# Optimization experiments

Measured on AMD Instinct MI355X. Metric: run time of the kernel, lower is better.

## Reference

```python
import jax, jax.numpy as jnp
import numpy as np

B, S, D, H, DFF = 2, 2048, 1024, 16, 4096
HD = D // H
EPS = 1e-5


def setup_inputs() -> dict:
    key = jax.random.key(0)
    ks = jax.random.split(key, 8)
    s = lambda fan_in: 1.0 / np.sqrt(fan_in)
    return {
        "x": jax.random.normal(ks[0], (B, S, D), jnp.float32),
        "ln1_g": jnp.ones((D,), jnp.float32),
        "ln1_b": jnp.zeros((D,), jnp.float32),
        "Wq": jax.random.normal(ks[1], (D, D), jnp.float32) * s(D),
        "Wk": jax.random.normal(ks[2], (D, D), jnp.float32) * s(D),
        "Wv": jax.random.normal(ks[3], (D, D), jnp.float32) * s(D),
        "Wo": jax.random.normal(ks[4], (D, D), jnp.float32) * s(D),
        "bo": jnp.zeros((D,), jnp.float32),
        "ln2_g": jnp.ones((D,), jnp.float32),
        "ln2_b": jnp.zeros((D,), jnp.float32),
        "W1": jax.random.normal(ks[5], (D, DFF), jnp.float32) * s(D),
        "b1": jnp.zeros((DFF,), jnp.float32),
        "W2": jax.random.normal(ks[6], (DFF, D), jnp.float32) * s(DFF),
        "b2": jnp.zeros((D,), jnp.float32),
    }


def _layernorm(x, g, b):
    mu = jnp.mean(x, axis=-1, keepdims=True)
    var = jnp.var(x, axis=-1, keepdims=True)
    return (x - mu) * jax.lax.rsqrt(var + EPS) * g + b


def reference(x, ln1_g, ln1_b, Wq, Wk, Wv, Wo, bo, ln2_g, ln2_b, W1, b1, W2, b2):
    # --- pre-LN + causal multi-head attention + residual ---
    h = _layernorm(x, ln1_g, ln1_b)
    q = (h @ Wq).reshape(B, S, H, HD).transpose(0, 2, 1, 3)  # [B,H,S,hd]
    k = (h @ Wk).reshape(B, S, H, HD).transpose(0, 2, 1, 3)
    v = (h @ Wv).reshape(B, S, H, HD).transpose(0, 2, 1, 3)
    scores = jnp.einsum("bhqd,bhkd->bhqk", q, k) / jnp.sqrt(jnp.float32(HD))
    causal = jnp.triu(jnp.ones((S, S), bool), k=1)  # True above diagonal -> masked
    scores = jnp.where(causal, -jnp.inf, scores)
    attn = jax.nn.softmax(scores, axis=-1)  # dropout is identity at inference
    ctx = jnp.einsum("bhqk,bhkd->bhqd", attn, v)
    ctx = ctx.transpose(0, 2, 1, 3).reshape(B, S, D)
    x = x + ctx @ Wo + bo
    # --- pre-LN + MLP + residual ---
    h = _layernorm(x, ln2_g, ln2_b)
    h = jax.nn.gelu(h @ W1 + b1, approximate=False)  # torch nn.GELU default = exact
    x = x + h @ W2 + b2
    return x
```

## Files before the change

### kernel.cpp

```cpp
#include <hip/hip_runtime.h>
#include <hip/hip_bf16.h>
#include <math.h>

using bf16 = __hip_bfloat16;
typedef short bf16x8 __attribute__((ext_vector_type(8)));
typedef float f32x4 __attribute__((ext_vector_type(4)));

static constexpr int B = 2, S = 2048, D = 1024, H = 16, HD = 64, DFF = 4096;
static constexpr int NR = B * S;
static constexpr int DQ = 3072;
static constexpr float EPS = 1e-5f;

__device__ __forceinline__ bf16 f2b(float v) { return __float2bfloat16(v); }

typedef __attribute__((address_space(1))) const void* gp1_t;
typedef __attribute__((address_space(3))) void* sp3_t;
__device__ __forceinline__ void gld_lds16(const bf16* g, bf16* l) {
    __builtin_amdgcn_global_load_lds((gp1_t)(const void*)g, (sp3_t)(void*)l, 16, 0, 0);
}

__global__ __launch_bounds__(256) void convT_kernel(const float* __restrict__ src,
                                                    bf16* __restrict__ dst,
                                                    int K, int N) {
    __shared__ float tile[64][65];
    const int k0 = blockIdx.x * 64, n0 = blockIdx.y * 64;
    const int tid = threadIdx.x;
    const int r = tid >> 4, c = (tid & 15) * 4;
#pragma unroll
    for (int rr = 0; rr < 64; rr += 16) {
        float4 v = *(const float4*)&src[(size_t)(k0 + r + rr) * N + n0 + c];
        tile[r + rr][c] = v.x; tile[r + rr][c + 1] = v.y;
        tile[r + rr][c + 2] = v.z; tile[r + rr][c + 3] = v.w;
    }
    __syncthreads();
    const int n = tid >> 2, ks = (tid & 3) * 16;
    union { bf16 h[16]; int4 v2[2]; } o;
#pragma unroll
    for (int i = 0; i < 16; ++i) o.h[i] = f2b(tile[ks + i][n]);
    bf16* dp = &dst[(size_t)(n0 + n) * K + k0 + ks];
    *(int4*)dp = o.v2[0];
    *(int4*)(dp + 8) = o.v2[1];
}

__global__ __launch_bounds__(256) void ln_kernel(const float* __restrict__ x,
                                                 const float* __restrict__ g,
                                                 const float* __restrict__ b,
                                                 bf16* __restrict__ out) {
    const int row = blockIdx.x;
    const int tid = threadIdx.x;
    const float4 v4 = ((const float4*)(x + (size_t)row * D))[tid];
    float v[4] = {v4.x, v4.y, v4.z, v4.w};
    float s = v[0] + v[1] + v[2] + v[3];
    float sq = v[0] * v[0] + v[1] * v[1] + v[2] * v[2] + v[3] * v[3];
#pragma unroll
    for (int off = 32; off >= 1; off >>= 1) {
        s += __shfl_xor(s, off);
        sq += __shfl_xor(sq, off);
    }
    __shared__ float ssum[4], ssq[4];
    const int wave = tid >> 6;
    if ((tid & 63) == 0) { ssum[wave] = s; ssq[wave] = sq; }
    __syncthreads();
    s = ssum[0] + ssum[1] + ssum[2] + ssum[3];
    sq = ssq[0] + ssq[1] + ssq[2] + ssq[3];
    const float mu = s * (1.0f / D);
    const float var = sq * (1.0f / D) - mu * mu;
    const float rstd = rsqrtf(var + EPS);
    bf16* orow = out + (size_t)row * D;
#pragma unroll
    for (int i = 0; i < 4; ++i) {
        const int c = tid * 4 + i;
        orow[c] = f2b((v[i] - mu) * rstd * g[c] + b[c]);
    }
}

template <int EPI>
__global__ __launch_bounds__(512) void gemm256(const bf16* __restrict__ A,
                                               const bf16* __restrict__ Bt,
                                               const float* __restrict__ bias,
                                               bf16* __restrict__ C,
                                               int M, int N, int K) {
    constexpr int ASZ = 256 * 32, BSZ = 128 * 32;
    constexpr int CST = 128 + 8;
    __shared__ __align__(16) bf16 smem[2 * (ASZ + BSZ)];

    const int Mtiles = M / 256;
    const int p = blockIdx.x;
    const int tm = p % Mtiles;
    const int tn = p / Mtiles;
    const int tid = threadIdx.x;
    const int wave = tid >> 6, lane = tid & 63;
    const int wm = wave >> 1, wn = wave & 1;
    const int quad = lane >> 4, l16 = lane & 15;

    f32x4 acc[4][4];
#pragma unroll
    for (int i = 0; i < 4; ++i)
#pragma unroll
        for (int j = 0; j < 4; ++j) acc[i][j] = (f32x4){0.f, 0.f, 0.f, 0.f};

    const int s_row = tid >> 2, s_seg = (tid & 3) * 8;
    const bf16* ApLo = A + (size_t)(tm * 256 + s_row) * K + s_seg;
    const size_t K128 = (size_t)128 * K;
    const bf16* Bp = Bt + (size_t)(tn * 128 + s_row) * K + s_seg;

    gld_lds16(ApLo, smem + tid * 8);
    gld_lds16(ApLo + K128, smem + (512 + tid) * 8);
    gld_lds16(Bp, smem + 2 * ASZ + tid * 8);
    ApLo += 32;
    Bp += 32;

    const int nk = K / 32;
    for (int kt = 0; kt < nk; ++kt) {
        const int cur = kt & 1, nxt = cur ^ 1;
        bf16* Acur = smem + cur * ASZ;
        bf16* Bcur = smem + 2 * ASZ + cur * BSZ;
        __syncthreads();
        if (kt + 1 < nk) {
            bf16* Anxt = smem + nxt * ASZ;
            bf16* Bnxt = smem + 2 * ASZ + nxt * BSZ;
            gld_lds16(ApLo, Anxt + tid * 8);
            gld_lds16(ApLo + K128, Anxt + (512 + tid) * 8);
            gld_lds16(Bp, Bnxt + tid * 8);
            ApLo += 32;
            Bp += 32;
        }

        bf16x8 aF[4], bF[4];
#pragma unroll
        for (int mt = 0; mt < 4; ++mt)
            aF[mt] = *(const bf16x8*)(Acur + (wm * 64 + mt * 16 + l16) * 32 + quad * 8);
#pragma unroll
        for (int nt = 0; nt < 4; ++nt)
            bF[nt] = *(const bf16x8*)(Bcur + (wn * 64 + nt * 16 + l16) * 32 + quad * 8);
#pragma unroll
        for (int mt = 0; mt < 4; ++mt)
#pragma unroll
            for (int nt = 0; nt < 4; ++nt)
                acc[mt][nt] = __builtin_amdgcn_mfma_f32_16x16x32_bf16(
                    aF[mt], bF[nt], acc[mt][nt], 0, 0, 0);
    }

#pragma unroll
    for (int hh = 0; hh < 2; ++hh) {
        __syncthreads();
        if ((wm >> 1) == hh) {
#pragma unroll
            for (int nt = 0; nt < 4; ++nt) {
                const int ccol = wn * 64 + nt * 16 + l16;
                float bv = 0.f;
                if (EPI == 2) bv = bias[tn * 128 + ccol];
#pragma unroll
                for (int mt = 0; mt < 4; ++mt) {
                    const int r0 = (wm & 1) * 64 + mt * 16 + quad * 4;
#pragma unroll
                    for (int j = 0; j < 4; ++j) {
                        float v = acc[mt][nt][j];
                        if (EPI == 2) {
                            v += bv;
                            v = 0.5f * v * (1.0f + erff(v * 0.70710678118654752f));
                        }
                        smem[(r0 + j) * CST + ccol] = f2b(v);
                    }
                }
            }
        }
        __syncthreads();
        bf16* crow = C + (size_t)(tm * 256 + hh * 128) * N + tn * 128;
#pragma unroll
        for (int i = 0; i < 4; ++i) {
            const int gid = i * 512 + tid;
            const int row = gid >> 4, c8 = gid & 15;
            const int4 val = *(const int4*)(smem + row * CST + c8 * 8);
            *(int4*)(crow + (size_t)row * N + c8 * 8) = val;
        }
    }
}

template <int EPI, int BN, int TPB>
__global__ __launch_bounds__(256) void gemm_bt(const bf16* __restrict__ A,
                                               const bf16* __restrict__ Bt,
                                               const float* __restrict__ bias,
                                               const float* __restrict__ res,
                                               void* __restrict__ Cv,
                                               int M, int N, int K) {
    constexpr int NTW = BN / 32;
    constexpr int ASZ = 128 * 32, BSZ = BN * 32;
    __shared__ __align__(16) bf16 smem[2 * (ASZ + BSZ)];

    const int Mtiles = M / 128;
    const int p = blockIdx.x;
    const int tm = p % Mtiles;
    const int tn0 = (p / Mtiles) * TPB;
    const int tid = threadIdx.x;
    const int wave = tid >> 6, lane = tid & 63;
    const int wm = wave >> 1, wn = wave & 1;
    const int quad = lane >> 4, l16 = lane & 15;

    const int s_row = tid >> 2, s_seg = (tid & 3) * 8;
    const size_t K64 = (size_t)64 * K;
    const int nk = K / 32;

    for (int tp = 0; tp < TPB; ++tp) {
        const int tn = tn0 + tp;
        if (tp) __syncthreads();

        f32x4 acc[4][NTW];
#pragma unroll
        for (int i = 0; i < 4; ++i)
#pragma unroll
            for (int j = 0; j < NTW; ++j) acc[i][j] = (f32x4){0.f, 0.f, 0.f, 0.f};

        const bf16* Ap = A + (size_t)(tm * 128 + s_row) * K + s_seg;
        const bf16* Bp = Bt + (size_t)(tn * BN + s_row) * K + s_seg;

        gld_lds16(Ap, smem + tid * 8);
        gld_lds16(Ap + K64, smem + (256 + tid) * 8);
        gld_lds16(Bp, smem + 2 * ASZ + tid * 8);
        if constexpr (BN == 128) gld_lds16(Bp + K64, smem + 2 * ASZ + (256 + tid) * 8);
        Ap += 32;
        Bp += 32;

        for (int kt = 0; kt < nk; ++kt) {
            const int cur = kt & 1, nxt = cur ^ 1;
            bf16* Acur = smem + cur * ASZ;
            bf16* Bcur = smem + 2 * ASZ + cur * BSZ;
            __syncthreads();
            if (kt + 1 < nk) {
                bf16* Anxt = smem + nxt * ASZ;
                bf16* Bnxt = smem + 2 * ASZ + nxt * BSZ;
                gld_lds16(Ap, Anxt + tid * 8);
                gld_lds16(Ap + K64, Anxt + (256 + tid) * 8);
                gld_lds16(Bp, Bnxt + tid * 8);
                if constexpr (BN == 128) gld_lds16(Bp + K64, Bnxt + (256 + tid) * 8);
                Ap += 32;
                Bp += 32;
            }

            bf16x8 aF[4], bF[NTW];
#pragma unroll
            for (int mt = 0; mt < 4; ++mt)
                aF[mt] = *(const bf16x8*)(Acur + (wm * 64 + mt * 16 + l16) * 32 + quad * 8);
#pragma unroll
            for (int nt = 0; nt < NTW; ++nt)
                bF[nt] = *(const bf16x8*)(Bcur + (wn * (BN / 2) + nt * 16 + l16) * 32 + quad * 8);
#pragma unroll
            for (int mt = 0; mt < 4; ++mt)
#pragma unroll
                for (int nt = 0; nt < NTW; ++nt)
                    acc[mt][nt] = __builtin_amdgcn_mfma_f32_16x16x32_bf16(
                        aF[mt], bF[nt], acc[mt][nt], 0, 0, 0);
        }

#pragma unroll
        for (int nt = 0; nt < NTW; ++nt) {
            const int col = tn * BN + wn * (BN / 2) + nt * 16 + l16;
            const float bv = bias[col];
#pragma unroll
            for (int mt = 0; mt < 4; ++mt) {
                const int row0 = tm * 128 + wm * 64 + mt * 16 + quad * 4;
#pragma unroll
                for (int j = 0; j < 4; ++j) {
                    const size_t idx = (size_t)(row0 + j) * N + col;
                    ((float*)Cv)[idx] = acc[mt][nt][j] + bv + res[idx];
                }
            }
        }
    }
}

__global__ __launch_bounds__(512) void fattn_kernel(const bf16* __restrict__ QKV,
                                                    bf16* __restrict__ ctx) {
    const int id = blockIdx.x;
    const int bh = id & 31;
    const int k = id >> 5;
    const int t = (k < 8) ? 15 - k : k - 8;
    const int b = bh >> 4, h = bh & (H - 1);
    const int tid = threadIdx.x;
    const int wave = tid >> 6, lane = tid & 63;
    const int quad = lane >> 4, l16 = lane & 15;
    const bf16* Qp = QKV + (size_t)b * S * DQ + h * HD;
    const bf16* Kp = Qp + D;
    const bf16* Vp = Qp + 2 * D;

    __shared__ __align__(16) bf16 Ks[2][64 * 64];
    __shared__ __align__(16) bf16 Vt[2][64][72];
    __shared__ __align__(16) bf16 Ps[128][76];

    const int keyA = tid >> 3, dsA = ((tid & 7) ^ (keyA & 7)) * 8;

    const int q0 = t * 128;
    const bf16* qg = Qp + (size_t)(q0 + wave * 16 + l16) * DQ + quad * 8;
    const bf16x8 aQ0 = *(const bf16x8*)(qg);
    const bf16x8 aQ1 = *(const bf16x8*)(qg + 32);

    f32x4 O[4];
#pragma unroll
    for (int nt = 0; nt < 4; ++nt) O[nt] = (f32x4){0.f, 0.f, 0.f, 0.f};
    float m[4] = {-3.0e38f, -3.0e38f, -3.0e38f, -3.0e38f};
    float l[4] = {0.f, 0.f, 0.f, 0.f};

    gld_lds16(Kp + (size_t)keyA * DQ + dsA, Ks[0] + tid * 8);
    {
        const bf16* vg = Vp + (size_t)lane * DQ + wave * 8;
        union { int4 v; bf16 hh[8]; } u;
        u.v = *(const int4*)vg;
#pragma unroll
        for (int i = 0; i < 8; ++i) Vt[0][wave * 8 + i][lane] = u.hh[i];
    }

    const int nch = 2 * t + 2;
    for (int c = 0; c < nch; ++c) {
        const int cur = c & 1, nxt = cur ^ 1;
        __syncthreads();
        union { int4 v; bf16 hh[8]; } u;
        if (c < nch - 1) {
            const int k1 = (c + 1) * 64;
            gld_lds16(Kp + (size_t)(k1 + keyA) * DQ + dsA, Ks[nxt] + tid * 8);
            u.v = *(const int4*)(Vp + (size_t)(k1 + lane) * DQ + wave * 8);
        }

        f32x4 sc[4];
#pragma unroll
        for (int nt = 0; nt < 4; ++nt) {
            const int r = nt * 16 + l16;
            const bf16x8 bK0 = *(const bf16x8*)(Ks[cur] + (r * 8 + (quad ^ (r & 7))) * 8);
            const bf16x8 bK1 = *(const bf16x8*)(Ks[cur] + (r * 8 + ((4 + quad) ^ (r & 7))) * 8);
            f32x4 z = (f32x4){0.f, 0.f, 0.f, 0.f};
            z = __builtin_amdgcn_mfma_f32_16x16x32_bf16(aQ0, bK0, z, 0, 0, 0);
            z = __builtin_amdgcn_mfma_f32_16x16x32_bf16(aQ1, bK1, z, 0, 0, 0);
            sc[nt] = z;
        }
#pragma unroll
        for (int nt = 0; nt < 4; ++nt)
#pragma unroll
            for (int j = 0; j < 4; ++j) sc[nt][j] *= 0.125f;
        if (c >= 2 * t) {
            const int kbase = (c - 2 * t) * 64;
#pragma unroll
            for (int nt = 0; nt < 4; ++nt) {
                const int rel_k = kbase + nt * 16 + l16;
#pragma unroll
                for (int j = 0; j < 4; ++j)
                    if (rel_k > wave * 16 + quad * 4 + j) sc[nt][j] = -3.0e38f;
            }
        }
        float al[4];
#pragma unroll
        for (int j = 0; j < 4; ++j) {
            float mx = fmaxf(fmaxf(sc[0][j], sc[1][j]), fmaxf(sc[2][j], sc[3][j]));
#pragma unroll
            for (int off = 1; off <= 8; off <<= 1) mx = fmaxf(mx, __shfl_xor(mx, off));
            const float mn = fmaxf(m[j], mx);
            al[j] = __expf(m[j] - mn);
            m[j] = mn;
            float rs = 0.f;
#pragma unroll
            for (int nt = 0; nt < 4; ++nt) {
                sc[nt][j] = __expf(sc[nt][j] - mn);
                rs += sc[nt][j];
            }
#pragma unroll
            for (int off = 1; off <= 8; off <<= 1) rs += __shfl_xor(rs, off);
            l[j] = l[j] * al[j] + rs;
        }
#pragma unroll
        for (int nt = 0; nt < 4; ++nt)
#pragma unroll
            for (int j = 0; j < 4; ++j)
                Ps[wave * 16 + quad * 4 + j][nt * 16 + l16] = f2b(sc[nt][j]);
        asm volatile("s_waitcnt lgkmcnt(0)" ::: "memory");
        const bf16x8 aP0 = *(const bf16x8*)&Ps[wave * 16 + l16][quad * 8];
        const bf16x8 aP1 = *(const bf16x8*)&Ps[wave * 16 + l16][32 + quad * 8];
#pragma unroll
        for (int nt = 0; nt < 4; ++nt)
#pragma unroll
            for (int j = 0; j < 4; ++j) O[nt][j] *= al[j];
#pragma unroll
        for (int nt = 0; nt < 4; ++nt) {
            const bf16x8 bV0 = *(const bf16x8*)&Vt[cur][nt * 16 + l16][quad * 8];
            const bf16x8 bV1 = *(const bf16x8*)&Vt[cur][nt * 16 + l16][32 + quad * 8];
            O[nt] = __builtin_amdgcn_mfma_f32_16x16x32_bf16(aP0, bV0, O[nt], 0, 0, 0);
            O[nt] = __builtin_amdgcn_mfma_f32_16x16x32_bf16(aP1, bV1, O[nt], 0, 0, 0);
        }
        if (c < nch - 1) {
#pragma unroll
            for (int i = 0; i < 8; ++i) Vt[nxt][wave * 8 + i][lane] = u.hh[i];
        }
    }

    const size_t hoC = (size_t)b * S * D + h * HD;
    float rl[4];
#pragma unroll
    for (int j = 0; j < 4; ++j) rl[j] = 1.0f / l[j];
#pragma unroll
    for (int nt = 0; nt < 4; ++nt)
#pragma unroll
        for (int j = 0; j < 4; ++j)
            ctx[hoC + (size_t)(q0 + wave * 16 + quad * 4 + j) * D + nt * 16 + l16] =
                f2b(O[nt][j] * rl[j]);
}

extern "C" void kernel_launch(void* const* d_in, const int* in_sizes, int n_in,
                              void* d_out, int out_size, void* d_ws, size_t ws_size,
                              hipStream_t stream) {
    const float* x     = (const float*)d_in[0];
    const float* ln1_g = (const float*)d_in[1];
    const float* ln1_b = (const float*)d_in[2];
    const float* Wq    = (const float*)d_in[3];
    const float* Wk    = (const float*)d_in[4];
    const float* Wv    = (const float*)d_in[5];
    const float* Wo    = (const float*)d_in[6];
    const float* bo    = (const float*)d_in[7];
    const float* ln2_g = (const float*)d_in[8];
    const float* ln2_b = (const float*)d_in[9];
    const float* W1    = (const float*)d_in[10];
    const float* b1    = (const float*)d_in[11];
    const float* W2    = (const float*)d_in[12];
    const float* b2    = (const float*)d_in[13];
    float* out = (float*)d_out;

    char* ws = (char*)d_ws;
    const size_t MB = (size_t)1 << 20;
    bf16* h     = (bf16*)(ws + 0 * MB);
    bf16* W1T   = (bf16*)(ws + 0 * MB);
    bf16* QKVb  = (bf16*)(ws + 8 * MB);
    bf16* hff   = (bf16*)(ws + 8 * MB);
    bf16* ctx   = (bf16*)(ws + 32 * MB);
    bf16* h2    = (bf16*)(ws + 40 * MB);
    bf16* WqkvT = (bf16*)(ws + 48 * MB);
    bf16* WoT   = (bf16*)(ws + 54 * MB);
    bf16* W2T   = (bf16*)(ws + 56 * MB);

    dim3 gt(16, 16);
    convT_kernel<<<gt, 256, 0, stream>>>(Wq, WqkvT,                 D, D);
    convT_kernel<<<gt, 256, 0, stream>>>(Wk, WqkvT + (size_t)D * D, D, D);
    convT_kernel<<<gt, 256, 0, stream>>>(Wv, WqkvT + (size_t)2 * D * D, D, D);
    convT_kernel<<<gt, 256, 0, stream>>>(Wo, WoT, D, D);
    convT_kernel<<<dim3(64, 16), 256, 0, stream>>>(W2, W2T, DFF, D);
    ln_kernel<<<NR, 256, 0, stream>>>(x, ln1_g, ln1_b, h);
    gemm256<0><<<(NR / 256) * (DQ / 128), 512, 0, stream>>>(
        h, WqkvT, nullptr, QKVb, NR, DQ, D);
    convT_kernel<<<dim3(16, 64), 256, 0, stream>>>(W1, W1T, D, DFF);
    fattn_kernel<<<dim3((S / 128) * B * H), 512, 0, stream>>>(QKVb, ctx);
    gemm_bt<1, 64, 1><<<(NR / 128) * (D / 64), 256, 0, stream>>>(
        ctx, WoT, bo, x, out, NR, D, D);
    ln_kernel<<<NR, 256, 0, stream>>>(out, ln2_g, ln2_b, h2);
    gemm256<2><<<(NR / 256) * (DFF / 128), 512, 0, stream>>>(
        h2, W1T, b1, hff, NR, DFF, D);
    gemm_bt<1, 64, 1><<<(NR / 128) * (D / 64), 256, 0, stream>>>(
        hff, W2T, b2, out, out, NR, D, DFF);
}
```

Before: 388.6 us.

## Transpose attention MFMA operands so each lane owns one query row

Swaps the A/B operands of the QK^T and PV MFMAs so the score and output accumulators hold the transposed tile, giving each lane a single query row. Softmax row max and sum then need one scalar per lane with two cross-quad shuffles instead of four rows with four shuffles each. P is written to LDS as packed 8-byte stores and the context output is stored as 8-byte vectors. The 1/sqrt(d) scale is folded into Q once, which adds one extra bf16 rounding of Q.

```diff
diff --git a/kernel.cpp b/kernel.cpp
--- a/kernel.cpp
+++ b/kernel.cpp
@@ -291,14 +291,22 @@
 
     const int q0 = t * 128;
     const bf16* qg = Qp + (size_t)(q0 + wave * 16 + l16) * DQ + quad * 8;
-    const bf16x8 aQ0 = *(const bf16x8*)(qg);
-    const bf16x8 aQ1 = *(const bf16x8*)(qg + 32);
+    union U8 { bf16 h[8]; bf16x8 v; };
+    U8 uq0, uq1;
+    uq0.v = *(const bf16x8*)(qg);
+    uq1.v = *(const bf16x8*)(qg + 32);
+#pragma unroll
+    for (int i = 0; i < 8; ++i) {
+        uq0.h[i] = f2b(__bfloat162float(uq0.h[i]) * 0.125f);
+        uq1.h[i] = f2b(__bfloat162float(uq1.h[i]) * 0.125f);
+    }
+    const bf16x8 aQ0 = uq0.v;
+    const bf16x8 aQ1 = uq1.v;
 
     f32x4 O[4];
 #pragma unroll
     for (int nt = 0; nt < 4; ++nt) O[nt] = (f32x4){0.f, 0.f, 0.f, 0.f};
-    float m[4] = {-3.0e38f, -3.0e38f, -3.0e38f, -3.0e38f};
-    float l[4] = {0.f, 0.f, 0.f, 0.f};
+    float rowm = -3.0e38f, rowl = 0.f;
 
     gld_lds16(Kp + (size_t)keyA * DQ + dsA, Ks[0] + tid * 8);
     {
@@ -327,61 +335,62 @@
             const bf16x8 bK0 = *(const bf16x8*)(Ks[cur] + (r * 8 + (quad ^ (r & 7))) * 8);
             const bf16x8 bK1 = *(const bf16x8*)(Ks[cur] + (r * 8 + ((4 + quad) ^ (r & 7))) * 8);
             f32x4 z = (f32x4){0.f, 0.f, 0.f, 0.f};
-            z = __builtin_amdgcn_mfma_f32_16x16x32_bf16(aQ0, bK0, z, 0, 0, 0);
-            z = __builtin_amdgcn_mfma_f32_16x16x32_bf16(aQ1, bK1, z, 0, 0, 0);
+            z = __builtin_amdgcn_mfma_f32_16x16x32_bf16(bK0, aQ0, z, 0, 0, 0);
+            z = __builtin_amdgcn_mfma_f32_16x16x32_bf16(bK1, aQ1, z, 0, 0, 0);
             sc[nt] = z;
         }
+        if (c >= 2 * t) {
+            const int kb0 = (c - 2 * t) * 64 + quad * 4;
+            const int qr = wave * 16 + l16;
+#pragma unroll
+            for (int nt = 0; nt < 4; ++nt)
+#pragma unroll
+                for (int j = 0; j < 4; ++j)
+                    if (kb0 + nt * 16 + j > qr) sc[nt][j] = -3.0e38f;
+        }
+        f32x4 mv;
+#pragma unroll
+        for (int j = 0; j < 4; ++j)
+            mv[j] = fmaxf(fmaxf(sc[0][j], sc[1][j]), fmaxf(sc[2][j], sc[3][j]));
+        float mx = fmaxf(fmaxf(mv[0], mv[1]), fmaxf(mv[2], mv[3]));
+        mx = fmaxf(mx, __shfl_xor(mx, 16));
+        mx = fmaxf(mx, __shfl_xor(mx, 32));
+        const float mn = fmaxf(rowm, mx);
+        const float alq = __expf(rowm - mn);
+        rowm = mn;
+        float rs = 0.f;
 #pragma unroll
         for (int nt = 0; nt < 4; ++nt)
 #pragma unroll
-            for (int j = 0; j < 4; ++j) sc[nt][j] *= 0.125f;
-        if (c >= 2 * t) {
-            const int kbase = (c - 2 * t) * 64;
-#pragma unroll
-            for (int nt = 0; nt < 4; ++nt) {
-                const int rel_k = kbase + nt * 16 + l16;
-#pragma unroll
-                for (int j = 0; j < 4; ++j)
-                    if (rel_k > wave * 16 + quad * 4 + j) sc[nt][j] = -3.0e38f;
-            }
-        }
-        float al[4];
-#pragma unroll
-        for (int j = 0; j < 4; ++j) {
-            float mx = fmaxf(fmaxf(sc[0][j], sc[1][j]), fmaxf(sc[2][j], sc[3][j]));
-#pragma unroll
-            for (int off = 1; off <= 8; off <<= 1) mx = fmaxf(mx, __shfl_xor(mx, off));
-            const float mn = fmaxf(m[j], mx);
-            al[j] = __expf(m[j] - mn);
-            m[j] = mn;
-            float rs = 0.f;
-#pragma unroll
-            for (int nt = 0; nt < 4; ++nt) {
+            for (int j = 0; j < 4; ++j) {
                 sc[nt][j] = __expf(sc[nt][j] - mn);
                 rs += sc[nt][j];
             }
-#pragma unroll
-            for (int off = 1; off <= 8; off <<= 1) rs += __shfl_xor(rs, off);
-            l[j] = l[j] * al[j] + rs;
-        }
+        rs += __shfl_xor(rs, 16);
+        rs += __shfl_xor(rs, 32);
+        rowl = rowl * alq + rs;
+
+        const int prow = wave * 16 + l16;
+#pragma unroll
+        for (int nt = 0; nt < 4; ++nt) {
+            union { bf16 h[4]; int2 v; } pk;
+#pragma unroll
+            for (int j = 0; j < 4; ++j) pk.h[j] = f2b(sc[nt][j]);
+            *(int2*)&Ps[prow][nt * 16 + quad * 4] = pk.v;
+        }
+        asm volatile("s_waitcnt lgkmcnt(0)" ::: "memory");
+        const bf16x8 aP0 = *(const bf16x8*)&Ps[prow][quad * 8];
+        const bf16x8 aP1 = *(const bf16x8*)&Ps[prow][32 + quad * 8];
 #pragma unroll
         for (int nt = 0; nt < 4; ++nt)
 #pragma unroll
-            for (int j = 0; j < 4; ++j)
-                Ps[wave * 16 + quad * 4 + j][nt * 16 + l16] = f2b(sc[nt][j]);
-        asm volatile("s_waitcnt lgkmcnt(0)" ::: "memory");
-        const bf16x8 aP0 = *(const bf16x8*)&Ps[wave * 16 + l16][quad * 8];
-        const bf16x8 aP1 = *(const bf16x8*)&Ps[wave * 16 + l16][32 + quad * 8];
-#pragma unroll
-        for (int nt = 0; nt < 4; ++nt)
-#pragma unroll
-            for (int j = 0; j < 4; ++j) O[nt][j] *= al[j];
+            for (int j = 0; j < 4; ++j) O[nt][j] *= alq;
 #pragma unroll
         for (int nt = 0; nt < 4; ++nt) {
             const bf16x8 bV0 = *(const bf16x8*)&Vt[cur][nt * 16 + l16][quad * 8];
             const bf16x8 bV1 = *(const bf16x8*)&Vt[cur][nt * 16 + l16][32 + quad * 8];
-            O[nt] = __builtin_amdgcn_mfma_f32_16x16x32_bf16(aP0, bV0, O[nt], 0, 0, 0);
-            O[nt] = __builtin_amdgcn_mfma_f32_16x16x32_bf16(aP1, bV1, O[nt], 0, 0, 0);
+            O[nt] = __builtin_amdgcn_mfma_f32_16x16x32_bf16(bV0, aP0, O[nt], 0, 0, 0);
+            O[nt] = __builtin_amdgcn_mfma_f32_16x16x32_bf16(bV1, aP1, O[nt], 0, 0, 0);
         }
         if (c < nch - 1) {
 #pragma unroll
@@ -389,16 +398,15 @@
         }
     }
 
-    const size_t hoC = (size_t)b * S * D + h * HD;
-    float rl[4];
-#pragma unroll
-    for (int j = 0; j < 4; ++j) rl[j] = 1.0f / l[j];
-#pragma unroll
-    for (int nt = 0; nt < 4; ++nt)
-#pragma unroll
-        for (int j = 0; j < 4; ++j)
-            ctx[hoC + (size_t)(q0 + wave * 16 + quad * 4 + j) * D + nt * 16 + l16] =
-                f2b(O[nt][j] * rl[j]);
+    const float rlq = 1.0f / rowl;
+    bf16* crow = ctx + (size_t)b * S * D + h * HD + (size_t)(q0 + wave * 16 + l16) * D;
+#pragma unroll
+    for (int nt = 0; nt < 4; ++nt) {
+        union { bf16 h[4]; int2 v; } o;
+#pragma unroll
+        for (int j = 0; j < 4; ++j) o.h[j] = f2b(O[nt][j] * rlq);
+        *(int2*)(crow + nt * 16 + quad * 4) = o.v;
+    }
 }
 
 extern "C" void kernel_launch(void* const* d_in, const int* in_sizes, int n_in,
```

Measured after the change: 360.2 us. 1.08x faster.
